# Kernel optimization log

Hardware: AMD Instinct MI355X
Metric: run time of the kernel (lower is better)

## Reference

```python
import jax, jax.numpy as jnp
import numpy as np

EMBED = 1024
HEADS = 16
HEAD_SIZE = 64


def setup_inputs() -> dict:
    key = jax.random.key(0)
    ks = jax.random.split(key, 6)
    B, T = 2, 2048
    s = EMBED ** -0.5
    x = jax.random.normal(ks[0], (B, T, EMBED), dtype=jnp.float32)
    Wk = jax.random.normal(ks[1], (EMBED, HEADS * HEAD_SIZE), dtype=jnp.float32) * s
    Wq = jax.random.normal(ks[2], (EMBED, HEADS * HEAD_SIZE), dtype=jnp.float32) * s
    Wv = jax.random.normal(ks[3], (EMBED, HEADS * HEAD_SIZE), dtype=jnp.float32) * s
    Wp = jax.random.normal(ks[4], (HEADS * HEAD_SIZE, EMBED), dtype=jnp.float32) * s
    bp = jax.random.normal(ks[5], (EMBED,), dtype=jnp.float32) * 0.01
    return {"x": x, "Wk": Wk, "Wq": Wq, "Wv": Wv, "Wp": Wp, "bp": bp}


def reference(x, Wk, Wq, Wv, Wp, bp):
    # x: [B, T, C]; dropout in eval mode (identity), matching inference semantics
    B, T, C = x.shape
    def split_heads(y):  # [B,T,H*Dh] -> [B,H,T,Dh]
        return y.reshape(B, T, HEADS, HEAD_SIZE).transpose(0, 2, 1, 3)
    q = split_heads(x @ Wq)
    k = split_heads(x @ Wk)
    v = split_heads(x @ Wv)
    scale = HEAD_SIZE ** -0.5
    wei = jnp.einsum('bhqd,bhkd->bhqk', q, k) * scale  # [B,H,T,T]
    causal = jnp.tril(jnp.ones((T, T), dtype=bool))
    wei = jnp.where(causal, wei, -jnp.inf)
    wei = jax.nn.softmax(wei, axis=-1)
    out = jnp.einsum('bhqk,bhkd->bhqd', wei, v)  # [B,H,T,Dh]
    out = out.transpose(0, 2, 1, 3).reshape(B, T, HEADS * HEAD_SIZE)
    return out @ Wp + bp
```

## Files before the change

### kernel.cpp

```cpp
#include <hip/hip_runtime.h>
#include <stdint.h>


typedef unsigned short bfu;
typedef unsigned int u32;
typedef short bf16x8 __attribute__((ext_vector_type(8)));
typedef float f32x4 __attribute__((ext_vector_type(4)));
typedef float f32x16 __attribute__((ext_vector_type(16)));

#define DEVI static __device__ __forceinline__

DEVI bfu f2bf(float f) {
  union { float f; unsigned u; } a; a.f = f;
  unsigned u = a.u;
  u += 0x7fffu + ((u >> 16) & 1u);
  return (bfu)(u >> 16);
}

DEVI float bf2f(bfu x) {
  union { u32 u; float f; } a; a.u = ((u32)x) << 16; return a.f;
}

DEVI void gld_lds16(const void* g, void* l) {
  __builtin_amdgcn_global_load_lds(
      (const __attribute__((address_space(1))) void*)g,
      (__attribute__((address_space(3))) void*)l, 16, 0, 0);
}

#define BAR_VM4()                                         \
  do {                                                    \
    asm volatile("s_waitcnt vmcnt(4)" ::: "memory");      \
    __builtin_amdgcn_s_barrier();                         \
    asm volatile("" ::: "memory");                        \
  } while (0)
#define BAR_VM2()                                         \
  do {                                                    \
    asm volatile("s_waitcnt vmcnt(2)" ::: "memory");      \
    __builtin_amdgcn_s_barrier();                         \
    asm volatile("" ::: "memory");                        \
  } while (0)
#define BAR_VM0()                                         \
  do {                                                    \
    asm volatile("s_waitcnt vmcnt(0)" ::: "memory");      \
    __builtin_amdgcn_s_barrier();                         \
    asm volatile("" ::: "memory");                        \
  } while (0)


__global__ __launch_bounds__(256) void conv_x(const float* __restrict__ x,
                                              bfu* __restrict__ xb) {
  const int n4 = (4096 * 1024) / 4;
  for (int i = blockIdx.x * 256 + threadIdx.x; i < n4; i += gridDim.x * 256) {
    float4 v = ((const float4*)x)[i];
    ushort4 p;
    p.x = f2bf(v.x); p.y = f2bf(v.y); p.z = f2bf(v.z); p.w = f2bf(v.w);
    ((ushort4*)xb)[i] = p;
  }
}

__global__ __launch_bounds__(256) void conv_w(
    const float* __restrict__ W0, const float* __restrict__ W1,
    const float* __restrict__ W2, const float* __restrict__ W3,
    bfu* __restrict__ T0, bfu* __restrict__ T1,
    bfu* __restrict__ T2, bfu* __restrict__ T3) {
  __shared__ bfu tile[64][65];
  const float* W; bfu* T;
  switch (blockIdx.z) {
    case 0:  W = W0; T = T0; break;
    case 1:  W = W1; T = T1; break;
    case 2:  W = W2; T = T2; break;
    default: W = W3; T = T3; break;
  }
  const int k0 = blockIdx.y * 64, n0 = blockIdx.x * 64;
  const int c = threadIdx.x & 63, r4 = threadIdx.x >> 6;
#pragma unroll
  for (int i = 0; i < 16; i++) {
    int row = r4 + i * 4;
    tile[row][c] = f2bf(W[(size_t)(k0 + row) * 1024 + n0 + c]);
  }
  __syncthreads();
#pragma unroll
  for (int i = 0; i < 16; i++) {
    int row = r4 + i * 4;
    T[(size_t)(n0 + row) * 1024 + k0 + c] = tile[c][row];
  }
}


__global__ __launch_bounds__(512) void gemm_qkv256(
    const bfu* __restrict__ A, const bfu* __restrict__ Bt,
    bfu* __restrict__ Qb, bfu* __restrict__ Kb, bfu* __restrict__ Vb) {
  __shared__ __align__(16) bfu LDS[2 * 32768];
  const int bid = blockIdx.x;
  const int xcd = bid & 7, i0 = bid >> 3;
  const int tx = i0 >> 1, ty = xcd * 2 + (i0 & 1);
  const int z = tx >> 2;
  const int m0 = ty * 256, n0g = tx * 256;
  const int tid = threadIdx.x, wave = tid >> 6, lane = tid & 63;
  const int wr = wave >> 2, wc = wave & 3;
  const int fr = lane & 15, fq = lane >> 4;
  const int rslot4 = fq ^ ((fr >> 1) & 3);

#define STAGE_HT(bufn, ktile, isB, kk)                                           \
  do {                                                                           \
    const bfu* srcb = (isB) ? Bt + (size_t)n0g * 1024 : A + (size_t)m0 * 1024;   \
    bfu* dstb = LDS + (bufn) * 32768 + ((isB) ? 16384 : 0) + (kk) * 8192;        \
    _Pragma("unroll")                                                            \
    for (int j_ = 0; j_ < 2; j_++) {                                             \
      int s_ = tid + j_ * 512;                                                   \
      int r_ = s_ >> 2, cg_ = (s_ & 3) ^ ((r_ >> 1) & 3);                        \
      gld_lds16(srcb + (size_t)r_ * 1024 + (ktile) * 64 + (kk) * 32 + cg_ * 8,   \
                dstb + s_ * 8);                                                  \
    }                                                                            \
  } while (0)

#define READ_B(kk)                                                               \
  _Pragma("unroll")                                                              \
  for (int n = 0; n < 4; n++)                                                    \
    bfv[n] = *(const bf16x8*)&bufc_p[16384 + (kk) * 8192 +                       \
              ((wc * 64 + n * 16 + fr) * 4 + rslot4) * 8];

#define READ_A(dst, mq, kk)                                                      \
  _Pragma("unroll")                                                              \
  for (int mm = 0; mm < 4; mm++)                                                 \
    dst[mm] = *(const bf16x8*)&bufc_p[(kk) * 8192 +                              \
              ((wr * 128 + ((mq) * 4 + mm) * 16 + fr) * 4 + rslot4) * 8];

#define MFMA_Q(afv, mq)                                                          \
  __builtin_amdgcn_s_setprio(1);                                                 \
  _Pragma("unroll")                                                              \
  for (int mm = 0; mm < 4; mm++)                                                 \
    _Pragma("unroll")                                                            \
    for (int n = 0; n < 4; n++)                                                  \
      acc[(mq) * 4 + mm][n] = __builtin_amdgcn_mfma_f32_16x16x32_bf16(           \
          afv[mm], bfv[n], acc[(mq) * 4 + mm][n], 0, 0, 0);                      \
  __builtin_amdgcn_s_setprio(0);

  f32x4 acc[8][4] = {};
  STAGE_HT(0, 0, 0, 0);
  STAGE_HT(0, 0, 1, 0);
  STAGE_HT(0, 0, 0, 1);
  STAGE_HT(0, 0, 1, 1);
  BAR_VM4();

  const int NT = 16;
  for (int t = 0; t < NT; t++) {
    const int more = (t + 1 < NT);
    const bfu* bufc_p = LDS + (t & 1) * 32768;
    const int bufn = (t & 1) ^ 1;
    bf16x8 bfv[4], afA[4], afB[4];
    READ_B(0);
    READ_A(afA, 0, 0);
    if (more) STAGE_HT(bufn, t + 1, 0, 0);
    MFMA_Q(afA, 0);
    READ_A(afB, 1, 0);
    if (more) STAGE_HT(bufn, t + 1, 1, 0);
    MFMA_Q(afB, 1);
    if (more) BAR_VM4();
    else      BAR_VM0();
    READ_B(1);
    READ_A(afA, 0, 1);
    if (more) STAGE_HT(bufn, t + 1, 0, 1);
    MFMA_Q(afA, 0);
    READ_A(afB, 1, 1);
    if (more) STAGE_HT(bufn, t + 1, 1, 1);
    MFMA_Q(afB, 1);
    BAR_VM4();
  }
#undef STAGE_HT
#undef READ_B
#undef READ_A
#undef MFMA_Q

  const float qs = (z == 0) ? 0.1803368801f : 1.0f;
#pragma unroll
  for (int mf = 0; mf < 8; mf++)
#pragma unroll
    for (int n = 0; n < 4; n++) {
      int r = m0 + wr * 128 + mf * 16 + fq * 4;
      int cwm = (tx & 3) * 256 + wc * 64 + n * 16 + fr;
      int b = r >> 11, tt = r & 2047, h = cwm >> 6, d = cwm & 63;
      if (z == 0) {
        size_t base = ((size_t)(b * 16 + h) * 2048 + tt) * 64 + d;
#pragma unroll
        for (int i = 0; i < 4; i++)
          Qb[base + (size_t)i * 64] = f2bf(acc[mf][n][i] * qs);
      } else if (z == 1) {
        size_t base = ((size_t)(b * 16 + h) * 2048 + tt) * 64 + d;
#pragma unroll
        for (int i = 0; i < 4; i++)
          Kb[base + (size_t)i * 64] = f2bf(acc[mf][n][i]);
      } else {
        size_t base = ((size_t)(b * 16 + h) * 64 + d) * 2048 + tt;
        ushort4 p;
        p.x = f2bf(acc[mf][n][0]); p.y = f2bf(acc[mf][n][1]);
        p.z = f2bf(acc[mf][n][2]); p.w = f2bf(acc[mf][n][3]);
        *(ushort4*)&Vb[base] = p;
      }
    }
}


__global__ __launch_bounds__(512) void gemm_proj(
    const bfu* __restrict__ A, const bfu* __restrict__ Bt,
    const float* __restrict__ bias, float* __restrict__ out) {
  __shared__ __align__(16) bfu LDS[2 * 16384];
  const int bid = blockIdx.x;
  const int xcd = bid & 7, i0 = bid >> 3;
  const int tx = i0 >> 2, ty = xcd * 4 + (i0 & 3);
  const int m0 = ty * 128, n0 = tx * 128;
  const int tid = threadIdx.x, wave = tid >> 6, lane = tid & 63;
  const int wr = wave >> 1, wc = wave & 1;
  const int fr = lane & 15, fq = lane >> 4;
  const int rslot4 = fq ^ ((fr >> 1) & 3);

#define STAGE_HT(bufn, ktile, isB, kk)                                           \
  do {                                                                           \
    const bfu* srcb = (isB) ? Bt + (size_t)n0 * 1024 : A + (size_t)m0 * 1024;    \
    bfu* dstb = LDS + (bufn) * 16384 + ((isB) ? 8192 : 0) + (kk) * 4096;         \
    int r_ = tid >> 2, cg_ = (tid & 3) ^ ((r_ >> 1) & 3);                        \
    gld_lds16(srcb + (size_t)r_ * 1024 + (ktile) * 64 + (kk) * 32 + cg_ * 8,     \
              dstb + tid * 8);                                                   \
  } while (0)

#define READ_B(kk)                                                               \
  _Pragma("unroll")                                                              \
  for (int n = 0; n < 4; n++)                                                    \
    bfv[n] = *(const bf16x8*)&bufc_p[8192 + (kk) * 4096 +                        \
              ((wc * 64 + n * 16 + fr) * 4 + rslot4) * 8];

#define READ_A(kk)                                                               \
  _Pragma("unroll")                                                              \
  for (int mm = 0; mm < 2; mm++)                                                 \
    af[mm] = *(const bf16x8*)&bufc_p[(kk) * 4096 +                               \
              ((wr * 32 + mm * 16 + fr) * 4 + rslot4) * 8];

#define MFMA_H(nq)                                                               \
  __builtin_amdgcn_s_setprio(1);                                                 \
  _Pragma("unroll")                                                              \
  for (int mm = 0; mm < 2; mm++)                                                 \
    _Pragma("unroll")                                                            \
    for (int n = 0; n < 2; n++)                                                  \
      acc[mm][(nq) * 2 + n] = __builtin_amdgcn_mfma_f32_16x16x32_bf16(           \
          af[mm], bfv[(nq) * 2 + n], acc[mm][(nq) * 2 + n], 0, 0, 0);            \
  __builtin_amdgcn_s_setprio(0);

  f32x4 acc[2][4] = {};
  STAGE_HT(0, 0, 0, 0);
  STAGE_HT(0, 0, 1, 0);
  STAGE_HT(0, 0, 0, 1);
  STAGE_HT(0, 0, 1, 1);
  BAR_VM2();

  const int NT = 16;
  for (int t = 0; t < NT; t++) {
    const int more = (t + 1 < NT);
    const bfu* bufc_p = LDS + (t & 1) * 16384;
    const int bufn = (t & 1) ^ 1;
    bf16x8 bfv[4], af[2];
    READ_B(0);
    READ_A(0);
    if (more) STAGE_HT(bufn, t + 1, 0, 0);
    MFMA_H(0);
    if (more) STAGE_HT(bufn, t + 1, 1, 0);
    MFMA_H(1);
    if (more) BAR_VM2();
    else      BAR_VM0();
    READ_B(1);
    READ_A(1);
    if (more) STAGE_HT(bufn, t + 1, 0, 1);
    MFMA_H(0);
    if (more) STAGE_HT(bufn, t + 1, 1, 1);
    MFMA_H(1);
    BAR_VM2();
  }
#undef STAGE_HT
#undef READ_B
#undef READ_A
#undef MFMA_H

#pragma unroll
  for (int mm = 0; mm < 2; mm++)
#pragma unroll
    for (int n = 0; n < 4; n++) {
      int r = m0 + wr * 32 + mm * 16 + fq * 4;
      int c = n0 + wc * 64 + n * 16 + fr;
      float bv = bias[c];
#pragma unroll
      for (int i = 0; i < 4; i++)
        out[(size_t)(r + i) * 1024 + c] = acc[mm][n][i] + bv;
    }
}


__global__ __launch_bounds__(256) void attn_fwd(
    const bfu* __restrict__ Q, const bfu* __restrict__ K,
    const bfu* __restrict__ Vt, bfu* __restrict__ Ob,
    bfu* __restrict__ PO, float* __restrict__ PM, float* __restrict__ PL) {
  __shared__ __align__(16) bfu Ks[3][4096];
  __shared__ __align__(16) bfu Vs[3][4096];
  const int bid = blockIdx.x;
  const int xcd = bid & 7, i0 = bid >> 3;
  const int slot = i0 >> 5, cuL = i0 & 31;
  const int head = cuL >> 3, cu8 = cuL & 7;
  const int hb = xcd * 4 + head;
  int qb, mode;
  if (slot < 2)      { qb = 15 - cu8; mode = slot + 1; }
  else if (cu8 < 4)  { if (slot == 3) return; qb = cu8; mode = 0; }
  else               { qb = cu8; mode = slot - 1; }
  const int kb0   = (mode == 2) ? (qb + 1) : 0;
  const int kbmax = (mode == 1) ? qb : (2 * qb + 1);
  const int tid = threadIdx.x, wave = tid >> 6, lane = tid & 63;
  const int q31 = lane & 31, hi = lane >> 5;
  const bfu* Qh = Q  + (size_t)hb * 2048 * 64;
  const bfu* Kh = K  + (size_t)hb * 2048 * 64;
  const bfu* Vh = Vt + (size_t)hb * 64 * 2048;
  const int b = hb >> 4, h = hb & 15;
  const int q0w = qb * 128 + wave * 32;
  const int qg = q0w + q31;

  const int r0 = tid >> 3, r1 = (256 + tid) >> 3;
  const int c0 = (tid & 7) ^ (r0 & 7), c1 = (tid & 7) ^ (r1 & 7);
#define STAGE_K(bufi, kbase)                                                          \
  do {                                                                                \
    gld_lds16(Kh + (size_t)((kbase) + r0) * 64 + c0 * 8, &Ks[bufi][tid * 8]);         \
    gld_lds16(Kh + (size_t)((kbase) + r1) * 64 + c1 * 8, &Ks[bufi][(256 + tid) * 8]); \
  } while (0)
#define STAGE_V(bufi, kbase)                                                          \
  do {                                                                                \
    gld_lds16(Vh + (size_t)r0 * 2048 + (kbase) + c0 * 8, &Vs[bufi][tid * 8]);         \
    gld_lds16(Vh + (size_t)r1 * 2048 + (kbase) + c1 * 8, &Vs[bufi][(256 + tid) * 8]); \
  } while (0)

  bf16x8 qv[4];
#pragma unroll
  for (int c = 0; c < 4; c++)
    qv[c] = *(const bf16x8*)&Qh[(size_t)(q0w + q31) * 64 + c * 16 + hi * 8];

  bf16x8 onesv;
#pragma unroll
  for (int j = 0; j < 8; j++) onesv[j] = (short)0x3F80;

  f32x16 o0 = {}, o1 = {}, lac = {};
  float m = -1e30f;

  STAGE_K(0, kb0 * 64);
  STAGE_V(0, kb0 * 64);
  STAGE_K(1, (kb0 + 1) * 64);
  STAGE_V(1, (kb0 + 1) * 64);
  BAR_VM4();

  for (int kb = kb0; kb <= kbmax; kb++) {
    const int idx = kb - kb0;
    const int cur = idx % 3, nxt = (idx + 2) % 3;
    const int pre = (kb + 2 <= kbmax);
    const int kbase = kb * 64;
    const int active = (kbase <= q0w + 31);
    const bfu* KsC = Ks[cur];
    const bfu* VsC = Vs[cur];
    if (pre) STAGE_K(nxt, (kb + 2) * 64);
    u32 W0[8], W1[8];
    if (active) {
      f32x16 s0 = {}, s1 = {};
#pragma unroll
      for (int c = 0; c < 4; c++) {
        const int g = 2 * c + hi;
        bf16x8 kf0 = *(const bf16x8*)&KsC[(q31 * 8 + (g ^ (q31 & 7))) * 8];
        bf16x8 kf1 = *(const bf16x8*)&KsC[((32 + q31) * 8 + (g ^ (q31 & 7))) * 8];
        s0 = __builtin_amdgcn_mfma_f32_32x32x16_bf16(kf0, qv[c], s0, 0, 0, 0);
        s1 = __builtin_amdgcn_mfma_f32_32x32x16_bf16(kf1, qv[c], s1, 0, 0, 0);
      }
      if (kbase + 63 > q0w) {
#pragma unroll
        for (int r = 0; r < 16; r++) {
          int krow = (r & 3) + 8 * (r >> 2) + 4 * hi;
          if (kbase + krow > qg)      s0[r] = -1e30f;
          if (kbase + 32 + krow > qg) s1[r] = -1e30f;
        }
      }
      float pm = s0[0];
#pragma unroll
      for (int r = 1; r < 16; r++) pm = fmaxf(pm, s0[r]);
#pragma unroll
      for (int r = 0; r < 16; r++) pm = fmaxf(pm, s1[r]);
      pm = fmaxf(pm, __shfl_xor(pm, 32));
      if (!__all(pm <= m + 8.0f)) {
        float mn = fmaxf(m, pm);
        float al = __builtin_amdgcn_exp2f(m - mn);
        m = mn;
#pragma unroll
        for (int r = 0; r < 16; r++) {
          float alq = __shfl(al, (r & 3) + 8 * (r >> 2) + 4 * hi);
          o0[r] *= alq; o1[r] *= alq; lac[r] *= alq;
        }
      }
#pragma unroll
      for (int w = 0; w < 8; w++) {
        float a0 = __builtin_amdgcn_exp2f(s0[2 * w] - m);
        float a1 = __builtin_amdgcn_exp2f(s0[2 * w + 1] - m);
        asm("v_cvt_pk_bf16_f32 %0, %1, %2" : "=v"(W0[w]) : "v"(a0), "v"(a1));
        float b0 = __builtin_amdgcn_exp2f(s1[2 * w] - m);
        float b1 = __builtin_amdgcn_exp2f(s1[2 * w + 1] - m);
        asm("v_cvt_pk_bf16_f32 %0, %1, %2" : "=v"(W1[w]) : "v"(b0), "v"(b1));
      }
    }
    if (pre) STAGE_V(nxt, (kb + 2) * 64);
    if (active) {
      __builtin_amdgcn_s_setprio(1);
#pragma unroll
      for (int c = 0; c < 4; c++) {
        const u32* Wsel = (c < 2) ? W0 : W1;
        const int w0 = 4 * (c & 1);
        u32 t0 = Wsel[w0],     t2 = Wsel[w0 + 2];
        u32 t1 = Wsel[w0 + 1], t3 = Wsel[w0 + 3];
        asm("v_permlane32_swap_b32 %0, %1" : "+v"(t0), "+v"(t2));
        asm("v_permlane32_swap_b32 %0, %1" : "+v"(t1), "+v"(t3));
        union { u32 u[4]; bf16x8 v; } pa;
        pa.u[0] = t0; pa.u[1] = t1; pa.u[2] = t2; pa.u[3] = t3;
        const int g = 2 * c + hi;
        bf16x8 vb0 = *(const bf16x8*)&VsC[(q31 * 8 + (g ^ (q31 & 7))) * 8];
        bf16x8 vb1 = *(const bf16x8*)&VsC[((32 + q31) * 8 + (g ^ (q31 & 7))) * 8];
        o0  = __builtin_amdgcn_mfma_f32_32x32x16_bf16(pa.v, vb0,   o0,  0, 0, 0);
        o1  = __builtin_amdgcn_mfma_f32_32x32x16_bf16(pa.v, vb1,   o1,  0, 0, 0);
        lac = __builtin_amdgcn_mfma_f32_32x32x16_bf16(pa.v, onesv, lac, 0, 0, 0);
      }
      __builtin_amdgcn_s_setprio(0);
    }
    if (pre) BAR_VM4();
    else     BAR_VM0();
  }
#undef STAGE_K
#undef STAGE_V

  if (mode == 0) {
#pragma unroll
    for (int r = 0; r < 16; r++) {
      int t = q0w + (r & 3) + 8 * (r >> 2) + 4 * hi;
      float inv = 1.0f / lac[r];
      size_t base = (size_t)(b * 2048 + t) * 1024 + h * 64;
      Ob[base + q31]      = f2bf(o0[r] * inv);
      Ob[base + 32 + q31] = f2bf(o1[r] * inv);
    }
  } else {
    const int p = (hb * 12 + (qb - 4)) * 2 + (mode - 1);
    bfu*   po = PO + (size_t)p * 8192;
    float* pmv = PM + p * 128;
    float* plv = PL + p * 128;
    pmv[wave * 32 + q31] = m;
#pragma unroll
    for (int r = 0; r < 16; r++) {
      int rm = (r & 3) + 8 * (r >> 2) + 4 * hi;
      plv[wave * 32 + rm] = lac[r];
      po[(wave * 32 + rm) * 64 + q31]      = f2bf(o0[r]);
      po[(wave * 32 + rm) * 64 + 32 + q31] = f2bf(o1[r]);
    }
  }
}

__global__ __launch_bounds__(256) void attn_comb(
    const bfu* __restrict__ PO, const float* __restrict__ PM,
    const float* __restrict__ PL, bfu* __restrict__ Ob) {
  const int g = blockIdx.x;
  const int hb = g / 12, j = g % 12, qb = j + 4;
  const int b = hb >> 4, h = hb & 15;
  const int p0 = g * 2, p1 = p0 + 1;
  const int tid = threadIdx.x;
  const int r = tid >> 1, ch = tid & 1;
  float m0 = PM[p0 * 128 + r], m1 = PM[p1 * 128 + r];
  float l0 = PL[p0 * 128 + r], l1 = PL[p1 * 128 + r];
  float ms = fmaxf(m0, m1);
  float f0 = __builtin_amdgcn_exp2f(m0 - ms);
  float f1 = __builtin_amdgcn_exp2f(m1 - ms);
  float inv = 1.0f / (l0 * f0 + l1 * f1);
  const bfu* a0 = PO + (size_t)p0 * 8192 + r * 64 + ch * 32;
  const bfu* a1 = PO + (size_t)p1 * 8192 + r * 64 + ch * 32;
  const int t = qb * 128 + r;
  bfu* ob = Ob + (size_t)(b * 2048 + t) * 1024 + h * 64 + ch * 32;
#pragma unroll
  for (int k = 0; k < 4; k++) {
    bf16x8 v0 = *(const bf16x8*)(a0 + k * 8);
    bf16x8 v1 = *(const bf16x8*)(a1 + k * 8);
    bf16x8 vo;
#pragma unroll
    for (int e = 0; e < 8; e++) {
      float acc = bf2f((bfu)(unsigned short)v0[e]) * f0 +
                  bf2f((bfu)(unsigned short)v1[e]) * f1;
      vo[e] = (short)f2bf(acc * inv);
    }
    *(bf16x8*)(ob + k * 8) = vo;
  }
}


extern "C" void kernel_launch(void* const* d_in, const int* in_sizes, int n_in,
                              void* d_out, int out_size, void* d_ws, size_t ws_size,
                              hipStream_t stream) {
  const float* x  = (const float*)d_in[0];
  const float* Wk = (const float*)d_in[1];
  const float* Wq = (const float*)d_in[2];
  const float* Wv = (const float*)d_in[3];
  const float* Wp = (const float*)d_in[4];
  const float* bp = (const float*)d_in[5];
  char* ws = (char*)d_ws;
  bfu* xb  = (bfu*)(ws);
  bfu* Wqt = (bfu*)(ws + ( 8u << 20));
  bfu* Wkt = (bfu*)(ws + (10u << 20));
  bfu* Wvt = (bfu*)(ws + (12u << 20));
  bfu* Wpt = (bfu*)(ws + (14u << 20));
  bfu* Qb  = (bfu*)(ws + (16u << 20));
  bfu* Kb  = (bfu*)(ws + (24u << 20));
  bfu* Vb  = (bfu*)(ws + (32u << 20));
  bfu* Ab  = (bfu*)(ws + (40u << 20));
  bfu*   PO = (bfu*)(ws);
  float* PM = (float*)(ws + (13u << 20));
  float* PL = (float*)(ws + (13u << 20) + (512u << 10));
  float* out = (float*)d_out;

  conv_x<<<1024, 256, 0, stream>>>(x, xb);
  conv_w<<<dim3(16, 16, 4), 256, 0, stream>>>(Wq, Wk, Wv, Wp, Wqt, Wkt, Wvt, Wpt);
  gemm_qkv256<<<192, 512, 0, stream>>>(xb, Wqt, Qb, Kb, Vb);
  attn_fwd<<<1024, 256, 0, stream>>>(Qb, Kb, Vb, Ab, PO, PM, PL);
  attn_comb<<<384, 256, 0, stream>>>(PO, PM, PL, Ab);
  gemm_proj<<<256, 512, 0, stream>>>(Ab, Wpt, bp, out);
}
```

Measured before the change: 113.4 us.

## Process two key tiles per barrier with four-deep LDS ring buffer

The attention loop now handles two 64-key tiles per iteration from a 4-slot K/V LDS ring, in place of one tile per iteration with a 3-slot ring. Prefetch of the next two tiles is issued during the first tile's compute, and a single full vmcnt(0) barrier is taken per pair. The aim is to halve barrier and sync overhead per tile. In exchange the prefetch depth within each pair is shallower, and LDS use grows from 48KB to 64KB, which may reduce occupancy.

```diff
diff --git a/kernel.cpp b/kernel.cpp
--- a/kernel.cpp
+++ b/kernel.cpp
@@ -297,8 +297,8 @@
     const bfu* __restrict__ Q, const bfu* __restrict__ K,
     const bfu* __restrict__ Vt, bfu* __restrict__ Ob,
     bfu* __restrict__ PO, float* __restrict__ PM, float* __restrict__ PL) {
-  __shared__ __align__(16) bfu Ks[3][4096];
-  __shared__ __align__(16) bfu Vs[3][4096];
+  __shared__ __align__(16) bfu Ks[4][4096];
+  __shared__ __align__(16) bfu Vs[4][4096];
   const int bid = blockIdx.x;
   const int xcd = bid & 7, i0 = bid >> 3;
   const int slot = i0 >> 5, cuL = i0 & 31;
@@ -344,91 +344,106 @@
   f32x16 o0 = {}, o1 = {}, lac = {};
   float m = -1e30f;
 
+#define TILE64(kbase_, KsC_, VsC_, HOOK1, HOOK2, HOOK3)                               \
+  do {                                                                                \
+    const int kbase = (kbase_);                                                       \
+    const bfu* KsC = (KsC_);                                                          \
+    const bfu* VsC = (VsC_);                                                          \
+    const int active = (kbase <= q0w + 31);                                           \
+    HOOK1;                                                                            \
+    u32 W0[8], W1[8];                                                                 \
+    if (active) {                                                                     \
+      f32x16 s0 = {}, s1 = {};                                                        \
+      _Pragma("unroll")                                                               \
+      for (int c = 0; c < 4; c++) {                                                   \
+        const int g = 2 * c + hi;                                                     \
+        bf16x8 kf0 = *(const bf16x8*)&KsC[(q31 * 8 + (g ^ (q31 & 7))) * 8];           \
+        bf16x8 kf1 = *(const bf16x8*)&KsC[((32 + q31) * 8 + (g ^ (q31 & 7))) * 8];    \
+        s0 = __builtin_amdgcn_mfma_f32_32x32x16_bf16(kf0, qv[c], s0, 0, 0, 0);        \
+        s1 = __builtin_amdgcn_mfma_f32_32x32x16_bf16(kf1, qv[c], s1, 0, 0, 0);        \
+      }                                                                               \
+      if (kbase + 63 > q0w) {                                                         \
+        _Pragma("unroll")                                                             \
+        for (int r = 0; r < 16; r++) {                                                \
+          int krow = (r & 3) + 8 * (r >> 2) + 4 * hi;                                 \
+          if (kbase + krow > qg)      s0[r] = -1e30f;                                 \
+          if (kbase + 32 + krow > qg) s1[r] = -1e30f;                                 \
+        }                                                                             \
+      }                                                                               \
+      float pm = s0[0];                                                               \
+      _Pragma("unroll")                                                               \
+      for (int r = 1; r < 16; r++) pm = fmaxf(pm, s0[r]);                             \
+      _Pragma("unroll")                                                               \
+      for (int r = 0; r < 16; r++) pm = fmaxf(pm, s1[r]);                             \
+      pm = fmaxf(pm, __shfl_xor(pm, 32));                                             \
+      if (!__all(pm <= m + 8.0f)) {                                                   \
+        float mn = fmaxf(m, pm);                                                      \
+        float al = __builtin_amdgcn_exp2f(m - mn);                                    \
+        m = mn;                                                                       \
+        _Pragma("unroll")                                                             \
+        for (int r = 0; r < 16; r++) {                                                \
+          float alq = __shfl(al, (r & 3) + 8 * (r >> 2) + 4 * hi);                    \
+          o0[r] *= alq; o1[r] *= alq; lac[r] *= alq;                                  \
+        }                                                                             \
+      }                                                                               \
+      _Pragma("unroll")                                                               \
+      for (int w = 0; w < 8; w++) {                                                   \
+        float a0 = __builtin_amdgcn_exp2f(s0[2 * w] - m);                             \
+        float a1 = __builtin_amdgcn_exp2f(s0[2 * w + 1] - m);                         \
+        asm("v_cvt_pk_bf16_f32 %0, %1, %2" : "=v"(W0[w]) : "v"(a0), "v"(a1));         \
+        float b0 = __builtin_amdgcn_exp2f(s1[2 * w] - m);                             \
+        float b1 = __builtin_amdgcn_exp2f(s1[2 * w + 1] - m);                         \
+        asm("v_cvt_pk_bf16_f32 %0, %1, %2" : "=v"(W1[w]) : "v"(b0), "v"(b1));         \
+      }                                                                               \
+    }                                                                                 \
+    HOOK2;                                                                            \
+    if (active) {                                                                     \
+      __builtin_amdgcn_s_setprio(1);                                                  \
+      _Pragma("unroll")                                                               \
+      for (int c = 0; c < 4; c++) {                                                   \
+        const u32* Wsel = (c < 2) ? W0 : W1;                                          \
+        const int w0 = 4 * (c & 1);                                                   \
+        u32 t0 = Wsel[w0],     t2 = Wsel[w0 + 2];                                     \
+        u32 t1 = Wsel[w0 + 1], t3 = Wsel[w0 + 3];                                     \
+        asm("v_permlane32_swap_b32 %0, %1" : "+v"(t0), "+v"(t2));                     \
+        asm("v_permlane32_swap_b32 %0, %1" : "+v"(t1), "+v"(t3));                     \
+        union { u32 u[4]; bf16x8 v; } pa;                                             \
+        pa.u[0] = t0; pa.u[1] = t1; pa.u[2] = t2; pa.u[3] = t3;                       \
+        const int g = 2 * c + hi;                                                     \
+        bf16x8 vb0 = *(const bf16x8*)&VsC[(q31 * 8 + (g ^ (q31 & 7))) * 8];           \
+        bf16x8 vb1 = *(const bf16x8*)&VsC[((32 + q31) * 8 + (g ^ (q31 & 7))) * 8];    \
+        o0  = __builtin_amdgcn_mfma_f32_32x32x16_bf16(pa.v, vb0,   o0,  0, 0, 0);     \
+        o1  = __builtin_amdgcn_mfma_f32_32x32x16_bf16(pa.v, vb1,   o1,  0, 0, 0);     \
+        lac = __builtin_amdgcn_mfma_f32_32x32x16_bf16(pa.v, onesv, lac, 0, 0, 0);     \
+      }                                                                               \
+      __builtin_amdgcn_s_setprio(0);                                                  \
+    }                                                                                 \
+    HOOK3;                                                                            \
+  } while (0)
+
   STAGE_K(0, kb0 * 64);
   STAGE_V(0, kb0 * 64);
   STAGE_K(1, (kb0 + 1) * 64);
   STAGE_V(1, (kb0 + 1) * 64);
-  BAR_VM4();
-
-  for (int kb = kb0; kb <= kbmax; kb++) {
+  BAR_VM0();
+
+  for (int kb = kb0; kb <= kbmax; kb += 2) {
     const int idx = kb - kb0;
-    const int cur = idx % 3, nxt = (idx + 2) % 3;
-    const int pre = (kb + 2 <= kbmax);
-    const int kbase = kb * 64;
-    const int active = (kbase <= q0w + 31);
-    const bfu* KsC = Ks[cur];
-    const bfu* VsC = Vs[cur];
-    if (pre) STAGE_K(nxt, (kb + 2) * 64);
-    u32 W0[8], W1[8];
-    if (active) {
-      f32x16 s0 = {}, s1 = {};
-#pragma unroll
-      for (int c = 0; c < 4; c++) {
-        const int g = 2 * c + hi;
-        bf16x8 kf0 = *(const bf16x8*)&KsC[(q31 * 8 + (g ^ (q31 & 7))) * 8];
-        bf16x8 kf1 = *(const bf16x8*)&KsC[((32 + q31) * 8 + (g ^ (q31 & 7))) * 8];
-        s0 = __builtin_amdgcn_mfma_f32_32x32x16_bf16(kf0, qv[c], s0, 0, 0, 0);
-        s1 = __builtin_amdgcn_mfma_f32_32x32x16_bf16(kf1, qv[c], s1, 0, 0, 0);
-      }
-      if (kbase + 63 > q0w) {
-#pragma unroll
-        for (int r = 0; r < 16; r++) {
-          int krow = (r & 3) + 8 * (r >> 2) + 4 * hi;
-          if (kbase + krow > qg)      s0[r] = -1e30f;
-          if (kbase + 32 + krow > qg) s1[r] = -1e30f;
-        }
-      }
-      float pm = s0[0];
-#pragma unroll
-      for (int r = 1; r < 16; r++) pm = fmaxf(pm, s0[r]);
-#pragma unroll
-      for (int r = 0; r < 16; r++) pm = fmaxf(pm, s1[r]);
-      pm = fmaxf(pm, __shfl_xor(pm, 32));
-      if (!__all(pm <= m + 8.0f)) {
-        float mn = fmaxf(m, pm);
-        float al = __builtin_amdgcn_exp2f(m - mn);
-        m = mn;
-#pragma unroll
-        for (int r = 0; r < 16; r++) {
-          float alq = __shfl(al, (r & 3) + 8 * (r >> 2) + 4 * hi);
-          o0[r] *= alq; o1[r] *= alq; lac[r] *= alq;
-        }
-      }
-#pragma unroll
-      for (int w = 0; w < 8; w++) {
-        float a0 = __builtin_amdgcn_exp2f(s0[2 * w] - m);
-        float a1 = __builtin_amdgcn_exp2f(s0[2 * w + 1] - m);
-        asm("v_cvt_pk_bf16_f32 %0, %1, %2" : "=v"(W0[w]) : "v"(a0), "v"(a1));
-        float b0 = __builtin_amdgcn_exp2f(s1[2 * w] - m);
-        float b1 = __builtin_amdgcn_exp2f(s1[2 * w + 1] - m);
-        asm("v_cvt_pk_bf16_f32 %0, %1, %2" : "=v"(W1[w]) : "v"(b0), "v"(b1));
-      }
-    }
-    if (pre) STAGE_V(nxt, (kb + 2) * 64);
-    if (active) {
-      __builtin_amdgcn_s_setprio(1);
-#pragma unroll
-      for (int c = 0; c < 4; c++) {
-        const u32* Wsel = (c < 2) ? W0 : W1;
-        const int w0 = 4 * (c & 1);
-        u32 t0 = Wsel[w0],     t2 = Wsel[w0 + 2];
-        u32 t1 = Wsel[w0 + 1], t3 = Wsel[w0 + 3];
-        asm("v_permlane32_swap_b32 %0, %1" : "+v"(t0), "+v"(t2));
-        asm("v_permlane32_swap_b32 %0, %1" : "+v"(t1), "+v"(t3));
-        union { u32 u[4]; bf16x8 v; } pa;
-        pa.u[0] = t0; pa.u[1] = t1; pa.u[2] = t2; pa.u[3] = t3;
-        const int g = 2 * c + hi;
-        bf16x8 vb0 = *(const bf16x8*)&VsC[(q31 * 8 + (g ^ (q31 & 7))) * 8];
-        bf16x8 vb1 = *(const bf16x8*)&VsC[((32 + q31) * 8 + (g ^ (q31 & 7))) * 8];
-        o0  = __builtin_amdgcn_mfma_f32_32x32x16_bf16(pa.v, vb0,   o0,  0, 0, 0);
-        o1  = __builtin_amdgcn_mfma_f32_32x32x16_bf16(pa.v, vb1,   o1,  0, 0, 0);
-        lac = __builtin_amdgcn_mfma_f32_32x32x16_bf16(pa.v, onesv, lac, 0, 0, 0);
-      }
-      __builtin_amdgcn_s_setprio(0);
-    }
-    if (pre) BAR_VM4();
-    else     BAR_VM0();
-  }
+    const int bA = idx & 3, bB = (idx + 1) & 3;
+    const int b2 = (idx + 2) & 3, b3 = (idx + 3) & 3;
+    const int have1 = (kb + 1 <= kbmax);
+    const int pre2 = (kb + 2 <= kbmax), pre3 = (kb + 3 <= kbmax);
+    TILE64(kb * 64, Ks[bA], Vs[bA],
+           { if (pre2) STAGE_K(b2, (kb + 2) * 64); },
+           { if (pre2) STAGE_V(b2, (kb + 2) * 64);
+             if (pre3) STAGE_K(b3, (kb + 3) * 64); },
+           { if (pre3) STAGE_V(b3, (kb + 3) * 64); });
+    if (have1)
+      TILE64((kb + 1) * 64, Ks[bB], Vs[bB],
+             ((void)0), ((void)0), ((void)0));
+    BAR_VM0();
+  }
+#undef TILE64
 #undef STAGE_K
 #undef STAGE_V
 
```

Result: no change. 114.2 us (+0.7%).

## Retile QKV GEMM to 256x192 tiles for a 256-block grid

Applied to the files above, without the earlier changes.

Changes the fused QKV projection GEMM tile from 256x256 to 256x192 columns, giving 256 workgroups instead of 192 so the grid fills all 256 compute units. The B staging is reworked to load both k-halves in three loads per thread, the wait counts are adjusted, and the epilogue computes per-column which of Q/K/V it writes because tiles now straddle matrix boundaries. The trade is less reuse per tile (smaller N) and a per-element z branch in the epilogue.

```diff
diff --git a/kernel.cpp b/kernel.cpp
--- a/kernel.cpp
+++ b/kernel.cpp
@@ -27,24 +27,16 @@
       (__attribute__((address_space(3))) void*)l, 16, 0, 0);
 }
 
-#define BAR_VM4()                                         \
+#define BAR_VMN(N)                                        \
   do {                                                    \
-    asm volatile("s_waitcnt vmcnt(4)" ::: "memory");      \
+    asm volatile("s_waitcnt vmcnt(" #N ")" ::: "memory"); \
     __builtin_amdgcn_s_barrier();                         \
     asm volatile("" ::: "memory");                        \
   } while (0)
-#define BAR_VM2()                                         \
-  do {                                                    \
-    asm volatile("s_waitcnt vmcnt(2)" ::: "memory");      \
-    __builtin_amdgcn_s_barrier();                         \
-    asm volatile("" ::: "memory");                        \
-  } while (0)
-#define BAR_VM0()                                         \
-  do {                                                    \
-    asm volatile("s_waitcnt vmcnt(0)" ::: "memory");      \
-    __builtin_amdgcn_s_barrier();                         \
-    asm volatile("" ::: "memory");                        \
-  } while (0)
+#define BAR_VM5() BAR_VMN(5)
+#define BAR_VM4() BAR_VMN(4)
+#define BAR_VM2() BAR_VMN(2)
+#define BAR_VM0() BAR_VMN(0)
 
 
 __global__ __launch_bounds__(256) void conv_x(const float* __restrict__ x,
@@ -87,38 +79,47 @@
 }
 
 
-__global__ __launch_bounds__(512) void gemm_qkv256(
+__global__ __launch_bounds__(512) void gemm_qkv192(
     const bfu* __restrict__ A, const bfu* __restrict__ Bt,
     bfu* __restrict__ Qb, bfu* __restrict__ Kb, bfu* __restrict__ Vb) {
-  __shared__ __align__(16) bfu LDS[2 * 32768];
+  __shared__ __align__(16) bfu LDS[2 * 28672];
   const int bid = blockIdx.x;
   const int xcd = bid & 7, i0 = bid >> 3;
-  const int tx = i0 >> 1, ty = xcd * 2 + (i0 & 1);
-  const int z = tx >> 2;
-  const int m0 = ty * 256, n0g = tx * 256;
+  const int ty = xcd * 2 + (i0 & 1), tx = i0 >> 1;
+  const int m0 = ty * 256, n0g = tx * 192;
   const int tid = threadIdx.x, wave = tid >> 6, lane = tid & 63;
   const int wr = wave >> 2, wc = wave & 3;
   const int fr = lane & 15, fq = lane >> 4;
   const int rslot4 = fq ^ ((fr >> 1) & 3);
 
-#define STAGE_HT(bufn, ktile, isB, kk)                                           \
+#define STAGE_A(bufn, ktile, kk)                                                 \
   do {                                                                           \
-    const bfu* srcb = (isB) ? Bt + (size_t)n0g * 1024 : A + (size_t)m0 * 1024;   \
-    bfu* dstb = LDS + (bufn) * 32768 + ((isB) ? 16384 : 0) + (kk) * 8192;        \
     _Pragma("unroll")                                                            \
     for (int j_ = 0; j_ < 2; j_++) {                                             \
       int s_ = tid + j_ * 512;                                                   \
       int r_ = s_ >> 2, cg_ = (s_ & 3) ^ ((r_ >> 1) & 3);                        \
-      gld_lds16(srcb + (size_t)r_ * 1024 + (ktile) * 64 + (kk) * 32 + cg_ * 8,   \
-                dstb + s_ * 8);                                                  \
+      gld_lds16(A + (size_t)(m0 + r_) * 1024 + (ktile) * 64 + (kk) * 32 + cg_ * 8,\
+                LDS + (bufn) * 28672 + (kk) * 8192 + s_ * 8);                    \
     }                                                                            \
   } while (0)
+#define STAGE_B(bufn, ktile)                                                     \
+  do {                                                                           \
+    _Pragma("unroll")                                                            \
+    for (int j_ = 0; j_ < 3; j_++) {                                             \
+      int s_ = tid + j_ * 512;                                                   \
+      int kk_ = (s_ >= 768) ? 1 : 0;                                             \
+      int sp_ = s_ - kk_ * 768;                                                  \
+      int r_ = sp_ >> 2, cg_ = (sp_ & 3) ^ ((r_ >> 1) & 3);                      \
+      gld_lds16(Bt + (size_t)(n0g + r_) * 1024 + (ktile) * 64 + kk_ * 32 + cg_ * 8,\
+                LDS + (bufn) * 28672 + 16384 + s_ * 8);                          \
+    }                                                                            \
+  } while (0)
 
 #define READ_B(kk)                                                               \
   _Pragma("unroll")                                                              \
-  for (int n = 0; n < 4; n++)                                                    \
-    bfv[n] = *(const bf16x8*)&bufc_p[16384 + (kk) * 8192 +                       \
-              ((wc * 64 + n * 16 + fr) * 4 + rslot4) * 8];
+  for (int n = 0; n < 3; n++)                                                    \
+    bfv[n] = *(const bf16x8*)&bufc_p[16384 + (kk) * 6144 +                       \
+              ((wc * 48 + n * 16 + fr) * 4 + rslot4) * 8];
 
 #define READ_A(dst, mq, kk)                                                      \
   _Pragma("unroll")                                                              \
@@ -131,54 +132,55 @@
   _Pragma("unroll")                                                              \
   for (int mm = 0; mm < 4; mm++)                                                 \
     _Pragma("unroll")                                                            \
-    for (int n = 0; n < 4; n++)                                                  \
+    for (int n = 0; n < 3; n++)                                                  \
       acc[(mq) * 4 + mm][n] = __builtin_amdgcn_mfma_f32_16x16x32_bf16(           \
           afv[mm], bfv[n], acc[(mq) * 4 + mm][n], 0, 0, 0);                      \
   __builtin_amdgcn_s_setprio(0);
 
-  f32x4 acc[8][4] = {};
-  STAGE_HT(0, 0, 0, 0);
-  STAGE_HT(0, 0, 1, 0);
-  STAGE_HT(0, 0, 0, 1);
-  STAGE_HT(0, 0, 1, 1);
-  BAR_VM4();
+  f32x4 acc[8][3] = {};
+  STAGE_A(0, 0, 0);
+  STAGE_B(0, 0);
+  STAGE_A(0, 0, 1);
+  BAR_VM2();
 
   const int NT = 16;
   for (int t = 0; t < NT; t++) {
     const int more = (t + 1 < NT);
-    const bfu* bufc_p = LDS + (t & 1) * 32768;
+    const bfu* bufc_p = LDS + (t & 1) * 28672;
     const int bufn = (t & 1) ^ 1;
-    bf16x8 bfv[4], afA[4], afB[4];
+    bf16x8 bfv[3], afA[4], afB[4];
     READ_B(0);
     READ_A(afA, 0, 0);
-    if (more) STAGE_HT(bufn, t + 1, 0, 0);
+    if (more) STAGE_A(bufn, t + 1, 0);
     MFMA_Q(afA, 0);
     READ_A(afB, 1, 0);
-    if (more) STAGE_HT(bufn, t + 1, 1, 0);
+    if (more) STAGE_B(bufn, t + 1);
     MFMA_Q(afB, 1);
-    if (more) BAR_VM4();
+    if (more) BAR_VM5();
     else      BAR_VM0();
     READ_B(1);
     READ_A(afA, 0, 1);
-    if (more) STAGE_HT(bufn, t + 1, 0, 1);
+    if (more) STAGE_A(bufn, t + 1, 1);
     MFMA_Q(afA, 0);
     READ_A(afB, 1, 1);
-    if (more) STAGE_HT(bufn, t + 1, 1, 1);
     MFMA_Q(afB, 1);
-    BAR_VM4();
-  }
-#undef STAGE_HT
+    if (more) BAR_VM2();
+    else      BAR_VM0();
+  }
+#undef STAGE_A
+#undef STAGE_B
 #undef READ_B
 #undef READ_A
 #undef MFMA_Q
 
-  const float qs = (z == 0) ? 0.1803368801f : 1.0f;
+  const float qs = 0.1803368801f;
 #pragma unroll
   for (int mf = 0; mf < 8; mf++)
 #pragma unroll
-    for (int n = 0; n < 4; n++) {
+    for (int n = 0; n < 3; n++) {
       int r = m0 + wr * 128 + mf * 16 + fq * 4;
-      int cwm = (tx & 3) * 256 + wc * 64 + n * 16 + fr;
+      int C = n0g + wc * 48 + n * 16 + fr;
+      int z = C >> 10, cwm = C & 1023;
       int b = r >> 11, tt = r & 2047, h = cwm >> 6, d = cwm & 63;
       if (z == 0) {
         size_t base = ((size_t)(b * 16 + h) * 2048 + tt) * 64 + d;
@@ -518,7 +520,7 @@
 
   conv_x<<<1024, 256, 0, stream>>>(x, xb);
   conv_w<<<dim3(16, 16, 4), 256, 0, stream>>>(Wq, Wk, Wv, Wp, Wqt, Wkt, Wvt, Wpt);
-  gemm_qkv256<<<192, 512, 0, stream>>>(xb, Wqt, Qb, Kb, Vb);
+  gemm_qkv192<<<256, 512, 0, stream>>>(xb, Wqt, Qb, Kb, Vb);
   attn_fwd<<<1024, 256, 0, stream>>>(Qb, Kb, Vb, Ab, PO, PM, PL);
   attn_comb<<<384, 256, 0, stream>>>(PO, PM, PL, Ab);
   gemm_proj<<<256, 512, 0, stream>>>(Ab, Wpt, bp, out);
```

After: 111.4 us. No clear change (-1.8%).
